# Kernel optimization log

Measured on AMD Instinct MI355X. Metric: run time of the kernel, lower is better.

## Reference

```python
import jax, jax.numpy as jnp
import numpy as np

T, H, W, C, HD, K = 4, 128, 128, 256, 8, 9
F = C // HD


def setup_inputs() -> dict:
    key = jax.random.key(0)
    ks = jax.random.split(key, 6)
    x = jax.random.normal(ks[0], (T, H, W, C), jnp.float32)
    attn = jax.random.uniform(ks[1], (1, HD, T, H, W, K), jnp.float32)
    attn = attn / attn.sum(-1, keepdims=True)  # softmax-normalized neighbor weights
    # integer flow offsets (dt, dh, dw) in [-3, 3], as produced by non-local search
    flows = jax.random.randint(ks[2], (1, HD, T, H, W, K, 3), -3, 4, jnp.int32)
    v_w = jax.random.normal(ks[3], (C, C), jnp.float32) * (C ** -0.5)
    proj_w = jax.random.normal(ks[4], (C, C), jnp.float32) * (C ** -0.5)
    proj_b = jnp.zeros((C,), jnp.float32)
    return dict(x=x, attn=attn, flows=flows, v_w=v_w, proj_w=proj_w, proj_b=proj_b)


def reference(x, attn, flows, v_w, proj_w, proj_b):
    T, H, W, C = x.shape
    HD = attn.shape[1]
    F = C // HD
    # v projection, split heads: [T,H,W,HD,F]
    v = (x @ v_w.T).reshape(T, H, W, HD, F)
    fl = flows[0]  # [HD,T,H,W,K,3] integer offsets (dt, dh, dw)
    tt = jnp.clip(jnp.arange(T)[None, :, None, None, None] + fl[..., 0], 0, T - 1)
    hh = jnp.clip(jnp.arange(H)[None, None, :, None, None] + fl[..., 1], 0, H - 1)
    ww = jnp.clip(jnp.arange(W)[None, None, None, :, None] + fl[..., 2], 0, W - 1)
    hd = jnp.arange(HD)[:, None, None, None, None]
    # flow-guided non-local gather: [HD,T,H,W,K,F]
    gathered = v[tt, hh, ww, hd]
    # attention-weighted sum over K neighbors, merge heads: [T,H,W,C]
    out = jnp.einsum('dthwk,dthwkf->thwdf', attn[0], gathered).reshape(T, H, W, C)
    # output projection
    return out @ proj_w.T + proj_b
```

## Files before the change

### kernel.cpp

```cpp
#include <hip/hip_runtime.h>
#include <hip/hip_bf16.h>

namespace {

constexpr int T = 4, H = 128, W = 128, C = 256, HD = 8, K = 9, F = 32;
constexpr int M = T * H * W;

typedef __attribute__((ext_vector_type(8))) short short8v;
typedef __attribute__((ext_vector_type(4))) float f32x4;

__device__ __forceinline__ unsigned short f2bf(float f) {
  unsigned u = __float_as_uint(f);
  unsigned r = (u + 0x7fffu + ((u >> 16) & 1u)) >> 16;
  return (unsigned short)r;
}

__device__ __forceinline__ float bf2f(unsigned short u) {
  return __uint_as_float(((unsigned)u) << 16);
}

template <int ALAYOUT, bool OUT_F32>
__global__ __launch_bounds__(256) void mfma_gemm(
    const void* __restrict__ Aptr, const float* __restrict__ Bw,
    void* __restrict__ Cptr, const float* __restrict__ bias) {
  __shared__ unsigned short As[128][40];
  __shared__ unsigned short Bs[128][40];
  const int m0 = blockIdx.x * 128;
  const int n0 = blockIdx.y * 128;
  const int t = threadIdx.x;
  const int lane = t & 63;
  const int wid = t >> 6;
  const int wm = wid >> 1, wn = wid & 1;
  const int fr = lane & 15;
  const int kg = lane >> 4;

  f32x4 acc[4][4];
#pragma unroll
  for (int ni = 0; ni < 4; ++ni) {
    float b = 0.f;
    if (OUT_F32) b = bias[n0 + wn * 64 + ni * 16 + fr];
#pragma unroll
    for (int mi = 0; mi < 4; ++mi) {
      acc[mi][ni][0] = b; acc[mi][ni][1] = b;
      acc[mi][ni][2] = b; acc[mi][ni][3] = b;
    }
  }

  for (int k0 = 0; k0 < C; k0 += 32) {
    __syncthreads();
    if (ALAYOUT == 2) {
      const unsigned short* Ab = (const unsigned short*)Aptr;
      const size_t hb = (size_t)(k0 >> 5) * M * 32;
#pragma unroll
      for (int i = 0; i < 2; ++i) {
        const int flat = t + i * 256;
        const int row = flat >> 2, kc = (flat & 3) * 8;
        *(short8v*)&As[row][kc] =
            *(const short8v*)(Ab + hb + (size_t)(m0 + row) * 32 + kc);
      }
    } else {
      const float* Af = (const float*)Aptr;
#pragma unroll
      for (int i = 0; i < 4; ++i) {
        const int flat = t + i * 256;
        const int row = flat >> 3, kc = (flat & 7) * 4;
        const float4 v4 = *(const float4*)(Af + (size_t)(m0 + row) * C + k0 + kc);
        ushort4 o;
        o.x = f2bf(v4.x); o.y = f2bf(v4.y); o.z = f2bf(v4.z); o.w = f2bf(v4.w);
        *(ushort4*)&As[row][kc] = o;
      }
    }
#pragma unroll
    for (int i = 0; i < 4; ++i) {
      const int flat = t + i * 256;
      const int row = flat >> 3, kc = (flat & 7) * 4;
      const float4 v4 = *(const float4*)(Bw + (size_t)(n0 + row) * C + k0 + kc);
      ushort4 o;
      o.x = f2bf(v4.x); o.y = f2bf(v4.y); o.z = f2bf(v4.z); o.w = f2bf(v4.w);
      *(ushort4*)&Bs[row][kc] = o;
    }
    __syncthreads();
    short8v af[4], bfv[4];
#pragma unroll
    for (int mi = 0; mi < 4; ++mi)
      af[mi] = *(const short8v*)&As[wm * 64 + mi * 16 + fr][kg * 8];
#pragma unroll
    for (int ni = 0; ni < 4; ++ni)
      bfv[ni] = *(const short8v*)&Bs[wn * 64 + ni * 16 + fr][kg * 8];
#pragma unroll
    for (int mi = 0; mi < 4; ++mi)
#pragma unroll
      for (int ni = 0; ni < 4; ++ni)
        acc[mi][ni] = __builtin_amdgcn_mfma_f32_16x16x32_bf16(
            af[mi], bfv[ni], acc[mi][ni], 0, 0, 0);
  }

#pragma unroll
  for (int mi = 0; mi < 4; ++mi) {
#pragma unroll
    for (int ni = 0; ni < 4; ++ni) {
      const int gcol = n0 + wn * 64 + ni * 16 + fr;
#pragma unroll
      for (int r = 0; r < 4; ++r) {
        const int grow = m0 + wm * 64 + mi * 16 + kg * 4 + r;
        if (OUT_F32) {
          ((float*)Cptr)[(size_t)grow * C + gcol] = acc[mi][ni][r];
        } else {
          ((unsigned short*)Cptr)[(size_t)grow * C + gcol] = f2bf(acc[mi][ni][r]);
        }
      }
    }
  }
}

struct __attribute__((packed, aligned(4))) I4p { int a, b, c, d; };
struct __attribute__((packed, aligned(4))) I2p { int a, b; };
struct __attribute__((packed, aligned(4))) F4p { float a, b, c, d; };

__global__ __launch_bounds__(256, 4) void gather_lds_kernel(
    const unsigned short* __restrict__ v, const float* __restrict__ attn,
    const int* __restrict__ flows, unsigned short* __restrict__ agg2) {
  __shared__ unsigned short halo[4 * 14 * 14 * 32];
  const int nb = (blockIdx.x & 7) * 256 + (blockIdx.x >> 3);
  const int head = nb & 7;
  const int tile = nb >> 3;
  const int h0 = (tile >> 4) * 8;
  const int w0 = (tile & 15) * 8;
  const int tid = threadIdx.x;
  const int s = tid & 63;
  const int tq = tid >> 6;
  const int h = h0 + (s >> 3);
  const int w = w0 + (s & 7);
  const int m = (tq << 14) | (h << 7) | w;

  const int base = ((head << 16) | m) * K;
  const int fb = base * 3;
  const I4p f0 = *(const I4p*)(flows + fb + 0);
  const I4p f1 = *(const I4p*)(flows + fb + 4);
  const I4p f2 = *(const I4p*)(flows + fb + 8);
  const I4p f3 = *(const I4p*)(flows + fb + 12);
  const I4p f4 = *(const I4p*)(flows + fb + 16);
  const I4p f5 = *(const I4p*)(flows + fb + 20);
  const I2p f6 = *(const I2p*)(flows + fb + 24);
  const int f7 = flows[fb + 26];
  const F4p a0 = *(const F4p*)(attn + base + 0);
  const F4p a1 = *(const F4p*)(attn + base + 4);
  const float a2 = attn[base + 8];

  const unsigned short* vhead = v + head * F;
#pragma unroll
  for (int it = 0; it < 13; ++it) {
    const int pi = tid + it * 256;
    if (pi < 3136) {
      const int sliver = pi >> 2, j = pi & 3;
      const int tt = sliver / 196;
      const int rem = sliver - tt * 196;
      const int hh = rem / 14;
      const int ww = rem - hh * 14;
      const int hc = min(max(h0 - 3 + hh, 0), H - 1);
      const int wc = min(max(w0 - 3 + ww, 0), W - 1);
      const int sm = (tt << 14) | (hc << 7) | wc;
      const short8v piece = *(const short8v*)(vhead + (size_t)sm * C + j * 8);
      const int jj = j ^ (sliver & 3);
      *(short8v*)&halo[sliver * 32 + jj * 8] = piece;
    }
  }
  __syncthreads();

  const int d[27] = {f0.a, f0.b, f0.c, f0.d, f1.a, f1.b, f1.c, f1.d,
                     f2.a, f2.b, f2.c, f2.d, f3.a, f3.b, f3.c, f3.d,
                     f4.a, f4.b, f4.c, f4.d, f5.a, f5.b, f5.c, f5.d,
                     f6.a, f6.b, f7};
  const float aw[9] = {a0.a, a0.b, a0.c, a0.d, a1.a, a1.b, a1.c, a1.d, a2};
  int row[9];
#pragma unroll
  for (int k = 0; k < 9; ++k) {
    const int ts = min(max(tq + d[3 * k + 0], 0), T - 1);
    const int hs = min(max(h + d[3 * k + 1], 0), H - 1) - (h0 - 3);
    const int ws = min(max(w + d[3 * k + 2], 0), W - 1) - (w0 - 3);
    row[k] = (ts * 14 + hs) * 14 + ws;
  }

  float acc[32];
#pragma unroll
  for (int i = 0; i < 32; ++i) acc[i] = 0.f;
#pragma unroll
  for (int k = 0; k < 9; ++k) {
    const int rbase = row[k] * 32;
    const int rsw = row[k] & 3;
#pragma unroll
    for (int j = 0; j < 4; ++j) {
      const short8v p = *(const short8v*)&halo[rbase + (j ^ rsw) * 8];
#pragma unroll
      for (int e = 0; e < 8; ++e)
        acc[j * 8 + e] += aw[k] * bf2f((unsigned short)p[e]);
    }
  }

  unsigned short* dst = agg2 + ((size_t)head * M + m) * F;
#pragma unroll
  for (int j = 0; j < 4; ++j) {
    short8v o;
#pragma unroll
    for (int e = 0; e < 8; ++e) o[e] = (short)f2bf(acc[j * 8 + e]);
    *(short8v*)(dst + j * 8) = o;
  }
}

__global__ __launch_bounds__(256) void agg_proj_kernel(
    const unsigned short* __restrict__ v, const float* __restrict__ attn,
    const int* __restrict__ flows, const float* __restrict__ proj_w,
    const float* __restrict__ proj_b, float* __restrict__ out) {
  __shared__ float Agg[32][C];
  __shared__ float Bs[32][C];
  const int bid = blockIdx.x;
  const int t = bid >> 9;
  const int h0 = ((bid >> 5) & 15) * 8;
  const int w0 = (bid & 31) * 4;
  const int tid = threadIdx.x;

  const int g = tid >> 3;
  const int f4 = (tid & 7) * 4;
#pragma unroll
  for (int r = 0; r < 8; ++r) {
    const int pi = r * 32 + g;
    const int pos = pi >> 3;
    const int head = pi & 7;
    const int h = h0 + (pos >> 2);
    const int w = w0 + (pos & 3);
    const int base = (((head * T + t) * H + h) * W + w) * K;
    const int fbase = base * 3;
    float4 acc = {0.f, 0.f, 0.f, 0.f};
#pragma unroll
    for (int k = 0; k < K; ++k) {
      const int dt = flows[fbase + k * 3 + 0];
      const int dh = flows[fbase + k * 3 + 1];
      const int dw = flows[fbase + k * 3 + 2];
      const float aw = attn[base + k];
      const int tt = min(max(t + dt, 0), T - 1);
      const int hh = min(max(h + dh, 0), H - 1);
      const int ww = min(max(w + dw, 0), W - 1);
      const int mm = (tt * H + hh) * W + ww;
      const ushort4 r4 = *(const ushort4*)(v + (size_t)mm * C + head * F + f4);
      acc.x += aw * bf2f(r4.x);
      acc.y += aw * bf2f(r4.y);
      acc.z += aw * bf2f(r4.z);
      acc.w += aw * bf2f(r4.w);
    }
    *(float4*)&Agg[pos][head * F + f4] = acc;
  }
  __syncthreads();

  const int tx = tid & 31;
  const int ty = tid >> 5;
  float acc2[4][8];
  {
    const float4 b0 = *(const float4*)(proj_b + tx * 8);
    const float4 b1 = *(const float4*)(proj_b + tx * 8 + 4);
#pragma unroll
    for (int i = 0; i < 4; ++i) {
      acc2[i][0] = b0.x; acc2[i][1] = b0.y; acc2[i][2] = b0.z; acc2[i][3] = b0.w;
      acc2[i][4] = b1.x; acc2[i][5] = b1.y; acc2[i][6] = b1.z; acc2[i][7] = b1.w;
    }
  }
  for (int k0 = 0; k0 < C; k0 += 32) {
#pragma unroll
    for (int i = 0; i < 8; ++i) {
      const float4 w4 = *(const float4*)(proj_w + (size_t)tid * C + k0 + i * 4);
      Bs[i * 4 + 0][tid] = w4.x;
      Bs[i * 4 + 1][tid] = w4.y;
      Bs[i * 4 + 2][tid] = w4.z;
      Bs[i * 4 + 3][tid] = w4.w;
    }
    __syncthreads();
#pragma unroll 4
    for (int kk = 0; kk < 32; ++kk) {
      const float4 bb0 = *(const float4*)&Bs[kk][tx * 8];
      const float4 bb1 = *(const float4*)&Bs[kk][tx * 8 + 4];
      float a[4];
#pragma unroll
      for (int i = 0; i < 4; ++i) a[i] = Agg[ty * 4 + i][k0 + kk];
#pragma unroll
      for (int i = 0; i < 4; ++i) {
        acc2[i][0] += a[i] * bb0.x;
        acc2[i][1] += a[i] * bb0.y;
        acc2[i][2] += a[i] * bb0.z;
        acc2[i][3] += a[i] * bb0.w;
        acc2[i][4] += a[i] * bb1.x;
        acc2[i][5] += a[i] * bb1.y;
        acc2[i][6] += a[i] * bb1.z;
        acc2[i][7] += a[i] * bb1.w;
      }
    }
    __syncthreads();
  }
#pragma unroll
  for (int i = 0; i < 4; ++i) {
    const int pos = ty * 4 + i;
    const int h = h0 + (pos >> 2);
    const int w = w0 + (pos & 3);
    const int m = (t * H + h) * W + w;
    float4 o0, o1;
    o0.x = acc2[i][0]; o0.y = acc2[i][1]; o0.z = acc2[i][2]; o0.w = acc2[i][3];
    o1.x = acc2[i][4]; o1.y = acc2[i][5]; o1.z = acc2[i][6]; o1.w = acc2[i][7];
    *(float4*)(out + (size_t)m * C + tx * 8) = o0;
    *(float4*)(out + (size_t)m * C + tx * 8 + 4) = o1;
  }
}

}

extern "C" void kernel_launch(void* const* d_in, const int* in_sizes, int n_in,
                              void* d_out, int out_size, void* d_ws,
                              size_t ws_size, hipStream_t stream) {
  const float* x = (const float*)d_in[0];
  const float* attn = (const float*)d_in[1];
  const int* flows = (const int*)d_in[2];
  const float* v_w = (const float*)d_in[3];
  const float* proj_w = (const float*)d_in[4];
  const float* proj_b = (const float*)d_in[5];
  float* out = (float*)d_out;

  const size_t VBYTES = (size_t)M * C * 2;
  unsigned short* v = (unsigned short*)d_ws;

  dim3 g1(M / 128, C / 128);
  mfma_gemm<0, false><<<g1, 256, 0, stream>>>(x, v_w, v, nullptr);

  if (ws_size >= 2 * VBYTES) {
    unsigned short* agg2 = (unsigned short*)((char*)d_ws + VBYTES);
    gather_lds_kernel<<<2048, 256, 0, stream>>>(v, attn, flows, agg2);
    mfma_gemm<2, true><<<g1, 256, 0, stream>>>(agg2, proj_w, out, proj_b);
  } else {
    const int nblk = T * (H / 8) * (W / 4);
    agg_proj_kernel<<<nblk, 256, 0, stream>>>(v, attn, flows, proj_w, proj_b,
                                              out);
  }
}
```

Before: 100.6 us.

## Load gather halo via global_load_lds and split feature dim across 512 threads

The halo fill in the gather kernel now uses direct global-to-LDS loads (global_load_lds, 16 bytes each) instead of going through registers. The swizzle moves from the LDS destination index to the global source column, since the LDS address is fixed per wave. The block size doubles to 512 threads, and each output pixel's 32 features are split into two 16-feature halves handled by different threads. This halves the accumulator registers and adds parallelism, while also duplicating the flow and attention loads and the offset math per thread.

```diff
diff --git a/kernel.cpp b/kernel.cpp
--- a/kernel.cpp
+++ b/kernel.cpp
@@ -17,6 +17,12 @@
 
 __device__ __forceinline__ float bf2f(unsigned short u) {
   return __uint_as_float(((unsigned)u) << 16);
+}
+
+__device__ __forceinline__ void load_lds16(const void* g, void* l) {
+  __builtin_amdgcn_global_load_lds(
+      (const __attribute__((address_space(1))) void*)g,
+      (__attribute__((address_space(3))) void*)l, 16, 0, 0);
 }
 
 template <int ALAYOUT, bool OUT_F32>
@@ -117,7 +123,7 @@
 struct __attribute__((packed, aligned(4))) I2p { int a, b; };
 struct __attribute__((packed, aligned(4))) F4p { float a, b, c, d; };
 
-__global__ __launch_bounds__(256, 4) void gather_lds_kernel(
+__global__ __launch_bounds__(512, 6) void gather_lds_kernel(
     const unsigned short* __restrict__ v, const float* __restrict__ attn,
     const int* __restrict__ flows, unsigned short* __restrict__ agg2) {
   __shared__ unsigned short halo[4 * 14 * 14 * 32];
@@ -128,7 +134,9 @@
   const int w0 = (tile & 15) * 8;
   const int tid = threadIdx.x;
   const int s = tid & 63;
-  const int tq = tid >> 6;
+  const int tq = (tid >> 6) & 3;
+  const int fh = tid >> 8;
+  const int wv = tid >> 6;
   const int h = h0 + (s >> 3);
   const int w = w0 + (s & 7);
   const int m = (tq << 14) | (h << 7) | w;
@@ -149,21 +157,32 @@
 
   const unsigned short* vhead = v + head * F;
 #pragma unroll
-  for (int it = 0; it < 13; ++it) {
-    const int pi = tid + it * 256;
-    if (pi < 3136) {
-      const int sliver = pi >> 2, j = pi & 3;
-      const int tt = sliver / 196;
-      const int rem = sliver - tt * 196;
-      const int hh = rem / 14;
-      const int ww = rem - hh * 14;
-      const int hc = min(max(h0 - 3 + hh, 0), H - 1);
-      const int wc = min(max(w0 - 3 + ww, 0), W - 1);
-      const int sm = (tt << 14) | (hc << 7) | wc;
-      const short8v piece = *(const short8v*)(vhead + (size_t)sm * C + j * 8);
-      const int jj = j ^ (sliver & 3);
-      *(short8v*)&halo[sliver * 32 + jj * 8] = piece;
-    }
+  for (int it = 0; it < 6; ++it) {
+    const int pi = it * 512 + tid;
+    const int sliver = pi >> 2, j = pi & 3;
+    const int tt = sliver / 196;
+    const int rem = sliver - tt * 196;
+    const int hh = rem / 14;
+    const int ww = rem - hh * 14;
+    const int hc = min(max(h0 - 3 + hh, 0), H - 1);
+    const int wc = min(max(w0 - 3 + ww, 0), W - 1);
+    const int sm = (tt << 14) | (hc << 7) | wc;
+    const int jj = j ^ (sliver & 3);
+    load_lds16(vhead + (size_t)sm * C + jj * 8,
+               (char*)halo + (size_t)(it * 512 + wv * 64) * 16);
+  }
+  if (tid < 64) {
+    const int pi = 3072 + tid;
+    const int sliver = pi >> 2, j = pi & 3;
+    const int tt = sliver / 196;
+    const int rem = sliver - tt * 196;
+    const int hh = rem / 14;
+    const int ww = rem - hh * 14;
+    const int hc = min(max(h0 - 3 + hh, 0), H - 1);
+    const int wc = min(max(w0 - 3 + ww, 0), W - 1);
+    const int sm = (tt << 14) | (hc << 7) | wc;
+    const int jj = j ^ (sliver & 3);
+    load_lds16(vhead + (size_t)sm * C + jj * 8, (char*)halo + (size_t)3072 * 16);
   }
   __syncthreads();
 
@@ -181,29 +200,30 @@
     row[k] = (ts * 14 + hs) * 14 + ws;
   }
 
-  float acc[32];
-#pragma unroll
-  for (int i = 0; i < 32; ++i) acc[i] = 0.f;
+  float acc[16];
+#pragma unroll
+  for (int i = 0; i < 16; ++i) acc[i] = 0.f;
 #pragma unroll
   for (int k = 0; k < 9; ++k) {
     const int rbase = row[k] * 32;
     const int rsw = row[k] & 3;
 #pragma unroll
-    for (int j = 0; j < 4; ++j) {
+    for (int jl = 0; jl < 2; ++jl) {
+      const int j = fh * 2 + jl;
       const short8v p = *(const short8v*)&halo[rbase + (j ^ rsw) * 8];
 #pragma unroll
       for (int e = 0; e < 8; ++e)
-        acc[j * 8 + e] += aw[k] * bf2f((unsigned short)p[e]);
-    }
-  }
-
-  unsigned short* dst = agg2 + ((size_t)head * M + m) * F;
-#pragma unroll
-  for (int j = 0; j < 4; ++j) {
+        acc[jl * 8 + e] += aw[k] * bf2f((unsigned short)p[e]);
+    }
+  }
+
+  unsigned short* dst = agg2 + ((size_t)head * M + m) * F + fh * 16;
+#pragma unroll
+  for (int jl = 0; jl < 2; ++jl) {
     short8v o;
 #pragma unroll
-    for (int e = 0; e < 8; ++e) o[e] = (short)f2bf(acc[j * 8 + e]);
-    *(short8v*)(dst + j * 8) = o;
+    for (int e = 0; e < 8; ++e) o[e] = (short)f2bf(acc[jl * 8 + e]);
+    *(short8v*)(dst + jl * 8) = o;
   }
 }
 
@@ -329,7 +349,7 @@
 
   if (ws_size >= 2 * VBYTES) {
     unsigned short* agg2 = (unsigned short*)((char*)d_ws + VBYTES);
-    gather_lds_kernel<<<2048, 256, 0, stream>>>(v, attn, flows, agg2);
+    gather_lds_kernel<<<2048, 512, 0, stream>>>(v, attn, flows, agg2);
     mfma_gemm<2, true><<<g1, 256, 0, stream>>>(agg2, proj_w, out, proj_b);
   } else {
     const int nblk = T * (H / 8) * (W / 4);
```

Result: slower. 151.6 us (+50.7%).
